# Kernel tuning notes

Measured on AMD Instinct MI355X. Metric: run time of the kernel, lower is better.

The kernel has to match this reference:

```python
import jax, jax.numpy as jnp
import numpy as np

N, M, D, OUT, K, L = 2048, 64, 64, 64, 3, 3  # meta-nodes, subgraph-nodes, channels, out, hops, layers
EPS = 1e-5


def setup_inputs() -> dict:
    key = jax.random.key(0)
    ks = jax.random.split(key, 6)
    x = jax.random.normal(ks[0], (N, M, D), dtype=jnp.float32)
    adj = jax.random.randint(ks[1], (N, N), 0, 2, dtype=jnp.int32)        # meta-graph adjacency
    sub_adj = jax.random.randint(ks[2], (M, M), 0, 2, dtype=jnp.int32)    # per-node subgraph adjacency
    # GCNConv params: (num_layers, k+1 convs per layer, D, D)
    W_convs = jax.random.normal(ks[3], (L, K + 1, D, D), dtype=jnp.float32) / np.float32(np.sqrt(D))
    b_convs = jnp.zeros((L, K + 1, D), dtype=jnp.float32)
    # LayerNorm over the trailing (m, d) dims, per layer
    ln_gamma = jnp.ones((L, M, D), dtype=jnp.float32)
    ln_beta = jnp.zeros((L, M, D), dtype=jnp.float32)
    W_lin = jax.random.normal(ks[4], (M * D, OUT), dtype=jnp.float32) / np.float32(np.sqrt(M * D))
    b_lin = jnp.zeros((OUT,), dtype=jnp.float32)
    return dict(x=x, sub_adj=sub_adj, adj=adj, W_convs=W_convs, b_convs=b_convs,
                ln_gamma=ln_gamma, ln_beta=ln_beta, W_lin=W_lin, b_lin=b_lin)


def _gcn_norm(A):
    # symmetric GCN normalization with self loops: D^{-1/2} (A+I) D^{-1/2}
    A = A.astype(jnp.float32) + jnp.eye(A.shape[0], dtype=jnp.float32)
    dinv = jax.lax.rsqrt(A.sum(axis=1))  # degree >= 1 thanks to self loops
    return dinv[:, None] * A * dinv[None, :]


def reference(x, sub_adj, adj, W_convs, b_convs, ln_gamma, ln_beta, W_lin, b_lin):
    # precompute_adj: dense powers [A, A^2, ..., A^K] of the meta-graph adjacency
    A = adj.astype(jnp.float32)
    cached = [A]
    P = A
    for _ in range(K - 1):
        P = P @ A
        cached.append(P)

    Sn = _gcn_norm(sub_adj)  # (M, M) shared normalized subgraph propagation

    def gcn(h, W, b):
        # GCNConv over the subgraph (m) dimension: Sn @ (h W) + b, batched over n
        return jnp.einsum('uv,nvd->nud', Sn, h @ W) + b

    for l in range(L):
        h = gcn(x, W_convs[l, 0], b_convs[l, 0])  # L[0](x, sub_adj)
        x_i = x
        for i in range(K):
            # k-hop propagation over the meta graph: x_i <- A^i-power @ x_i
            x_i = jnp.einsum('nj,jmd->nmd', cached[i], x_i)
            h = h + gcn(x_i, W_convs[l, i + 1], b_convs[l, i + 1])
        # LayerNorm over trailing (m, d) dims, then ReLU
        mu = h.mean(axis=(1, 2), keepdims=True)
        var = h.var(axis=(1, 2), keepdims=True)
        x = (h - mu) * jax.lax.rsqrt(var + EPS) * ln_gamma[l] + ln_beta[l]
        x = jax.nn.relu(x)

    # final readout linear over flattened (m*d)
    out = x.reshape(N, M * D) @ W_lin + b_lin  # (N, OUT)
    return out
```

## Files before the change

kernel.cpp:

```cpp
#include <hip/hip_runtime.h>
#include <math.h>

#define NN 2048
#define MM 64
#define DD 64
#define MD 4096
#define NLAYER 3
#define EPS 1e-5f

typedef unsigned short u16;
typedef unsigned int u32;
typedef __attribute__((ext_vector_type(8))) short bf16x8;
typedef __attribute__((ext_vector_type(4))) float f32x4;

__device__ inline u16 f32_to_bf16(float f) {
    u32 u = __float_as_uint(f);
    u32 r = (u + 0x7FFFu + ((u >> 16) & 1u)) >> 16;
    return (u16)r;
}
__device__ inline float bf16_to_f32(u16 h) { return __uint_as_float((u32)h << 16); }
__device__ inline void split3(float f, u16& h, u16& l, u16& q) {
    h = f32_to_bf16(f); float r = f - bf16_to_f32(h);
    l = f32_to_bf16(r); r -= bf16_to_f32(l);
    q = f32_to_bf16(r);
}

__global__ __launch_bounds__(256) void aprep_kernel(const int* __restrict__ adj,
                                                    u16* __restrict__ Abf,
                                                    u16* __restrict__ ATbf) {
    __shared__ u16 T[64][65];
    const int r0 = blockIdx.y * 64, c0 = blockIdx.x * 64;
    const int tid = threadIdx.x;
#pragma unroll
    for (int e = 0; e < 16; ++e) {
        int idx = e * 256 + tid;
        int i = idx >> 6, j = idx & 63;
        int a = adj[(long)(r0 + i) * NN + c0 + j];
        u16 b = a ? (u16)0x3F80 : (u16)0;
        Abf[(long)(r0 + i) * NN + c0 + j] = b;
        T[i][j] = b;
    }
    __syncthreads();
#pragma unroll
    for (int e = 0; e < 16; ++e) {
        int idx = e * 256 + tid;
        int cc = idx >> 6, rr = idx & 63;
        ATbf[(long)(c0 + cc) * NN + r0 + rr] = T[rr][cc];
    }
}

__global__ __launch_bounds__(256) void snprep_kernel(const int* __restrict__ sub,
                                                     u16* __restrict__ SnS) {
    __shared__ float dinv[64];
    __shared__ float Snl[64][65];
    int tid = threadIdx.x;
    if (tid < 64) {
        float s = 1.f;
        for (int v = 0; v < 64; ++v) s += (float)sub[tid * 64 + v];
        dinv[tid] = 1.f / sqrtf(s);
    }
    __syncthreads();
    for (int t = tid; t < 4096; t += 256) {
        int u = t >> 6, v = t & 63;
        float a = (float)sub[t] + (u == v ? 1.f : 0.f);
        Snl[u][v] = dinv[u] * a * dinv[v];
    }
    __syncthreads();
    for (int u = tid * 2; u < tid * 2 + 2; ++u) {
        int row = u >> 3, c8 = u & 7;
        int su = (u ^ ((u >> 3) & 7)) * 8;
#pragma unroll
        for (int e = 0; e < 8; ++e) {
            u16 h, l, q; split3(Snl[row][c8 * 8 + e], h, l, q);
            SnS[su + e] = h;
            SnS[4096 + su + e] = l;
            SnS[8192 + su + e] = q;
        }
    }
}

__global__ __launch_bounds__(256) void wprep_kernel(const float* __restrict__ Wc,
                                                    u16* __restrict__ WtS) {
    __shared__ float Wl[64][65];
    const int cu = blockIdx.x, tid = threadIdx.x;
    const float* W = Wc + (size_t)cu * 4096;
    for (int t = tid; t < 4096; t += 256) Wl[t >> 6][t & 63] = W[t];
    __syncthreads();
    u16* dst = WtS + (size_t)cu * 3 * 4096;
    for (int u = tid * 2; u < tid * 2 + 2; ++u) {
        int d = u >> 3, c8 = u & 7;
        int su = (u ^ ((u >> 3) & 7)) * 8;
#pragma unroll
        for (int e = 0; e < 8; ++e) {
            u16 h, l, q; split3(Wl[c8 * 8 + e][d], h, l, q);
            dst[su + e] = h;
            dst[4096 + su + e] = l;
            dst[8192 + su + e] = q;
        }
    }
}

template <int S>
__global__ __launch_bounds__(256) void split_pow_kernel(const float* __restrict__ X,
                                                        u16* __restrict__ P, long n) {
    long i = (long)blockIdx.x * 256 + threadIdx.x;
    if (i >= n) return;
    float v = X[i];
#pragma unroll
    for (int s = 0; s < S; ++s) {
        u16 h = f32_to_bf16(v);
        P[(long)s * n + i] = h;
        v -= bf16_to_f32(h);
    }
}

__global__ __launch_bounds__(256) void split3t_kernel(const float* __restrict__ X,
                                                      u16* __restrict__ P, int R, int Cc) {
    __shared__ float T[64][65];
    const int r0 = blockIdx.y * 64, c0 = blockIdx.x * 64;
    const int tid = threadIdx.x;
#pragma unroll
    for (int e = 0; e < 16; ++e) {
        int idx = e * 256 + tid;
        int i = idx >> 6, j = idx & 63;
        T[i][j] = X[(long)(r0 + i) * Cc + c0 + j];
    }
    __syncthreads();
    const long planeStride = (long)R * Cc;
#pragma unroll
    for (int e = 0; e < 16; ++e) {
        int idx = e * 256 + tid;
        int cc = idx >> 6, rr = idx & 63;
        float v = T[rr][cc];
        u16 h, l, q; split3(v, h, l, q);
        long o = (long)(c0 + cc) * R + r0 + rr;
        P[o] = h;
        P[planeStride + o] = l;
        P[2 * planeStride + o] = q;
    }
}

template <int SP, int SQ, int SMAX>
__global__ __launch_bounds__(256) void gemm_pairs(const u16* __restrict__ Ap, long aStride,
                                                  const u16* __restrict__ Bp, long bStride,
                                                  float* __restrict__ C, int M, int N, int K) {
    __shared__ u16 lds[(SP + SQ) * 4096];
    const int tid = threadIdx.x;
    const int wave = tid >> 6, lane = tid & 63;
    const int nwg = gridDim.x * gridDim.y;
    int bid = blockIdx.y * gridDim.x + blockIdx.x;
    int sbid = (bid & 7) * (nwg >> 3) + (bid >> 3);
    const int bm = (sbid / gridDim.x) * 128, bn = (sbid % gridDim.x) * 128;
    const int wr = (wave >> 1) * 64, wc = (wave & 1) * 64;

    f32x4 acc[4][4];
#pragma unroll
    for (int i = 0; i < 4; ++i)
#pragma unroll
        for (int j = 0; j < 4; ++j) acc[i][j] = (f32x4){0.f, 0.f, 0.f, 0.f};

    const int kb16 = lane >> 4, lr = lane & 15;
    int aoff[4], boff[4];
#pragma unroll
    for (int mi = 0; mi < 4; ++mi) {
        int ua = (wr + mi * 16 + lr) * 4 + kb16;
        aoff[mi] = (ua ^ ((ua >> 3) & 7)) * 16;
        int ub = (wc + mi * 16 + lr) * 4 + kb16;
        boff[mi] = (ub ^ ((ub >> 3) & 7)) * 16;
    }
    auto stage = [&](int k0) {
#pragma unroll
        for (int u8 = 0; u8 < (SP + SQ) * 2; ++u8) {
            int uu = u8 * 4 + wave;
            int p = uu >> 3, i = uu & 7;
            int us = i * 64 + lane;
            int ulin = us ^ ((us >> 3) & 7);
            int r = ulin >> 2, kb = ulin & 3;
            const u16* src; int rowbase;
            if (p < SP) { src = Ap + (long)p * aStride; rowbase = bm; }
            else        { src = Bp + (long)(p - SP) * bStride; rowbase = bn; }
            const char* g = (const char*)src + ((long)(rowbase + r) * K + k0) * 2 + kb * 16;
            char* l = (char*)lds + p * 8192 + i * 1024 + lane * 16;
            __builtin_amdgcn_global_load_lds((const __attribute__((address_space(1))) void*)g,
                                             (__attribute__((address_space(3))) void*)l, 16, 0, 0);
        }
    };
    stage(0);
    __syncthreads();
    for (int k0 = 0; k0 < K; k0 += 32) {
        bf16x8 a[SP][4], b[SQ][4];
#pragma unroll
        for (int s = 0; s < SP; ++s)
#pragma unroll
            for (int mi = 0; mi < 4; ++mi)
                a[s][mi] = *(const bf16x8*)((const char*)lds + s * 8192 + aoff[mi]);
#pragma unroll
        for (int t = 0; t < SQ; ++t)
#pragma unroll
            for (int ni = 0; ni < 4; ++ni)
                b[t][ni] = *(const bf16x8*)((const char*)lds + (SP + t) * 8192 + boff[ni]);
        __syncthreads();
        if (k0 + 32 < K) stage(k0 + 32);
#pragma unroll
        for (int s = 0; s < SP; ++s)
#pragma unroll
            for (int t = 0; t < SQ; ++t)
                if (s + t <= SMAX) {
#pragma unroll
                    for (int mi = 0; mi < 4; ++mi)
#pragma unroll
                        for (int ni = 0; ni < 4; ++ni)
                            acc[mi][ni] = __builtin_amdgcn_mfma_f32_16x16x32_bf16(
                                a[s][mi], b[t][ni], acc[mi][ni], 0, 0, 0);
                }
        __syncthreads();
    }
#pragma unroll
    for (int mi = 0; mi < 4; ++mi)
#pragma unroll
        for (int ni = 0; ni < 4; ++ni)
#pragma unroll
            for (int j = 0; j < 4; ++j)
                C[(long)(bm + wr + mi * 16 + (lane >> 4) * 4 + j) * N + bn + wc + ni * 16 + lr] =
                    acc[mi][ni][j];
}

template <int NC, int MODE>
__global__ __launch_bounds__(256, 2) void gcn_conv_kernel(
    const float* __restrict__ X0, const float* __restrict__ X1,
    const float* __restrict__ X2, const float* __restrict__ X3,
    const u16* __restrict__ WtS,
    const float* __restrict__ bias,
    const u16* __restrict__ SnS,
    const float* __restrict__ gam, const float* __restrict__ bet,
    float* __restrict__ Hout) {
    __shared__ u16 lds[9 * 4096];
    __shared__ float redf[4];
    const int tid = threadIdx.x;
    const int wave = tid >> 6, lane = tid & 63;
    const int lr = lane & 15, lg = lane >> 4;
    const int n = blockIdx.x;
    const int TT = 0, WT = 3 * 4096, SN = 6 * 4096;

    {
        const char* src = (const char*)SnS;
        char* dst = (char*)lds + (size_t)SN * 2;
#pragma unroll
        for (int i = 0; i < 6; ++i)
            __builtin_amdgcn_global_load_lds(
                (const __attribute__((address_space(1))) void*)(src + (i * 256 + tid) * 16),
                (__attribute__((address_space(3))) void*)(dst + (i * 256 + tid) * 16), 16, 0, 0);
    }
    const float* Xc[4] = {X0, X1, X2, X3};
    f32x4 accH[4];
#pragma unroll
    for (int ni = 0; ni < 4; ++ni) accH[ni] = (f32x4){0.f, 0.f, 0.f, 0.f};

    for (int c = 0; c < NC; ++c) {
        __syncthreads();
        {
            const char* wsrc = (const char*)(WtS + (size_t)c * 3 * 4096);
            char* wdst = (char*)lds + (size_t)WT * 2;
#pragma unroll
            for (int i = 0; i < 6; ++i)
                __builtin_amdgcn_global_load_lds(
                    (const __attribute__((address_space(1))) void*)(wsrc + (i * 256 + tid) * 16),
                    (__attribute__((address_space(3))) void*)(wdst + (i * 256 + tid) * 16), 16, 0, 0);
        }
        const float* xp = Xc[c] + (size_t)n * 4096;
        bf16x8 xb[3][4][2];
#pragma unroll
        for (int ni = 0; ni < 4; ++ni)
#pragma unroll
            for (int ks = 0; ks < 2; ++ks) {
                int off = (ni * 16 + lr) * 64 + ks * 32 + lg * 8;
                f32x4 v0 = *(const f32x4*)(xp + off);
                f32x4 v1 = *(const f32x4*)(xp + off + 4);
#pragma unroll
                for (int e = 0; e < 8; ++e) {
                    float f = (e < 4) ? v0[e] : v1[e - 4];
                    u16 h, l, q; split3(f, h, l, q);
                    xb[0][ni][ks][e] = (short)h;
                    xb[1][ni][ks][e] = (short)l;
                    xb[2][ni][ks][e] = (short)q;
                }
            }
        __syncthreads();
        f32x4 accT[4];
#pragma unroll
        for (int ni = 0; ni < 4; ++ni) accT[ni] = (f32x4){0.f, 0.f, 0.f, 0.f};
#pragma unroll
        for (int ks = 0; ks < 2; ++ks) {
            bf16x8 aw[3];
#pragma unroll
            for (int s = 0; s < 3; ++s) {
                int u = (wave * 16 + lr) * 8 + ks * 4 + lg;
                aw[s] = *(const bf16x8*)(lds + WT + s * 4096 + (u ^ ((u >> 3) & 7)) * 8);
            }
#pragma unroll
            for (int ni = 0; ni < 4; ++ni) {
                accT[ni] = __builtin_amdgcn_mfma_f32_16x16x32_bf16(aw[0], xb[0][ni][ks], accT[ni], 0, 0, 0);
                accT[ni] = __builtin_amdgcn_mfma_f32_16x16x32_bf16(aw[0], xb[1][ni][ks], accT[ni], 0, 0, 0);
                accT[ni] = __builtin_amdgcn_mfma_f32_16x16x32_bf16(aw[1], xb[0][ni][ks], accT[ni], 0, 0, 0);
                accT[ni] = __builtin_amdgcn_mfma_f32_16x16x32_bf16(aw[1], xb[1][ni][ks], accT[ni], 0, 0, 0);
                accT[ni] = __builtin_amdgcn_mfma_f32_16x16x32_bf16(aw[2], xb[0][ni][ks], accT[ni], 0, 0, 0);
                accT[ni] = __builtin_amdgcn_mfma_f32_16x16x32_bf16(aw[0], xb[2][ni][ks], accT[ni], 0, 0, 0);
            }
        }
#pragma unroll
        for (int ni = 0; ni < 4; ++ni)
#pragma unroll
            for (int j = 0; j < 4; ++j) {
                int d = wave * 16 + lg * 4 + j;
                int v = ni * 16 + lr;
                u16 h, l, q; split3(accT[ni][j], h, l, q);
                int u = d * 8 + (v >> 3);
                int o = (u ^ ((u >> 3) & 7)) * 8 + (v & 7);
                lds[TT + o] = h;
                lds[TT + 4096 + o] = l;
                lds[TT + 8192 + o] = q;
            }
        __syncthreads();
#pragma unroll
        for (int ks = 0; ks < 2; ++ks) {
            bf16x8 as_[3];
#pragma unroll
            for (int s = 0; s < 3; ++s) {
                int u = (wave * 16 + lr) * 8 + ks * 4 + lg;
                as_[s] = *(const bf16x8*)(lds + SN + s * 4096 + (u ^ ((u >> 3) & 7)) * 8);
            }
#pragma unroll
            for (int ni = 0; ni < 4; ++ni) {
                bf16x8 bt[3];
#pragma unroll
                for (int t = 0; t < 3; ++t) {
                    int u = (ni * 16 + lr) * 8 + ks * 4 + lg;
                    bt[t] = *(const bf16x8*)(lds + TT + t * 4096 + (u ^ ((u >> 3) & 7)) * 8);
                }
                accH[ni] = __builtin_amdgcn_mfma_f32_16x16x32_bf16(as_[0], bt[0], accH[ni], 0, 0, 0);
                accH[ni] = __builtin_amdgcn_mfma_f32_16x16x32_bf16(as_[0], bt[1], accH[ni], 0, 0, 0);
                accH[ni] = __builtin_amdgcn_mfma_f32_16x16x32_bf16(as_[1], bt[0], accH[ni], 0, 0, 0);
                accH[ni] = __builtin_amdgcn_mfma_f32_16x16x32_bf16(as_[1], bt[1], accH[ni], 0, 0, 0);
                accH[ni] = __builtin_amdgcn_mfma_f32_16x16x32_bf16(as_[2], bt[0], accH[ni], 0, 0, 0);
                accH[ni] = __builtin_amdgcn_mfma_f32_16x16x32_bf16(as_[0], bt[2], accH[ni], 0, 0, 0);
            }
        }
#pragma unroll
        for (int ni = 0; ni < 4; ++ni) {
            float bv = bias[c * 64 + ni * 16 + lr];
            accH[ni][0] += bv; accH[ni][1] += bv; accH[ni][2] += bv; accH[ni][3] += bv;
        }
    }
    float* hp = Hout + (size_t)n * 4096;
    float val[4][4];
#pragma unroll
    for (int ni = 0; ni < 4; ++ni)
#pragma unroll
        for (int j = 0; j < 4; ++j) {
            int idx = (wave * 16 + lg * 4 + j) * 64 + ni * 16 + lr;
            float v = accH[ni][j];
            if (MODE == 0 || MODE == 2) v += hp[idx];
            val[ni][j] = v;
        }
    if (MODE == 0 || MODE == 1) {
#pragma unroll
        for (int ni = 0; ni < 4; ++ni)
#pragma unroll
            for (int j = 0; j < 4; ++j)
                hp[(wave * 16 + lg * 4 + j) * 64 + ni * 16 + lr] = val[ni][j];
        return;
    }
    float part = 0.f;
#pragma unroll
    for (int ni = 0; ni < 4; ++ni)
#pragma unroll
        for (int j = 0; j < 4; ++j) part += val[ni][j];
#pragma unroll
    for (int o = 32; o; o >>= 1) part += __shfl_down(part, o);
    if (lane == 0) redf[wave] = part;
    __syncthreads();
    float mean = (redf[0] + redf[1] + redf[2] + redf[3]) * (1.f / 4096.f);
    float p2 = 0.f;
#pragma unroll
    for (int ni = 0; ni < 4; ++ni)
#pragma unroll
        for (int j = 0; j < 4; ++j) {
            float d_ = val[ni][j] - mean;
            p2 += d_ * d_;
        }
#pragma unroll
    for (int o = 32; o; o >>= 1) p2 += __shfl_down(p2, o);
    __syncthreads();
    if (lane == 0) redf[wave] = p2;
    __syncthreads();
    float var = (redf[0] + redf[1] + redf[2] + redf[3]) * (1.f / 4096.f);
    float rstd = 1.f / sqrtf(var + EPS);
#pragma unroll
    for (int ni = 0; ni < 4; ++ni)
#pragma unroll
        for (int j = 0; j < 4; ++j) {
            int idx = (wave * 16 + lg * 4 + j) * 64 + ni * 16 + lr;
            float v = (val[ni][j] - mean) * rstd * gam[idx] + bet[idx];
            hp[idx] = v > 0.f ? v : 0.f;
        }
}

__global__ __launch_bounds__(256) void readout_kernel(const float* __restrict__ X,
                                                      const float* __restrict__ Wl,
                                                      const float* __restrict__ bl,
                                                      float* __restrict__ out) {
    const int n = blockIdx.x;
    const int o = threadIdx.x & 63, c = threadIdx.x >> 6;
    const float* xn = X + (size_t)n * MD;
    float s = 0.f;
    for (int i = c * 1024; i < (c + 1) * 1024; ++i) s += xn[i] * Wl[(size_t)i * 64 + o];
    __shared__ float red[4][64];
    red[c][o] = s;
    __syncthreads();
    if (c == 0) out[(size_t)n * 64 + o] = red[0][o] + red[1][o] + red[2][o] + red[3][o] + bl[o];
}

extern "C" void kernel_launch(void* const* d_in, const int* in_sizes, int n_in,
                              void* d_out, int out_size, void* d_ws, size_t ws_size,
                              hipStream_t stream) {
    const float* x     = (const float*)d_in[0];
    const int*   sub   = (const int*)d_in[1];
    const int*   adj   = (const int*)d_in[2];
    const float* Wc    = (const float*)d_in[3];
    const float* bc    = (const float*)d_in[4];
    const float* gamma = (const float*)d_in[5];
    const float* beta  = (const float*)d_in[6];
    const float* Wlin  = (const float*)d_in[7];
    const float* blin  = (const float*)d_in[8];
    float* out = (float*)d_out;

    char* w = (char*)d_ws;
    u16* Abf = (u16*)w;  w += (size_t)NN * NN * 2;
    u16* A2p = (u16*)w;  w += (size_t)2 * NN * NN * 2;
    u16* A3p = (u16*)w;  w += (size_t)3 * NN * NN * 2;
    u16* SnS = (u16*)w;  w += (size_t)3 * 4096 * 2;
    u16* WtS = (u16*)w;  w += (size_t)12 * 3 * 4096 * 2;
    u16* S   = (u16*)w;  w += (size_t)3 * NN * MD * 2;
    const size_t baseBytes = (size_t)(w - (char*)d_ws);
    const size_t ybytes = (size_t)NN * MD * 4;
    const bool fused = ws_size >= baseBytes + 4 * ybytes;
    u16* ATbf = S;
    float* A2f = (float*)((char*)S + (size_t)NN * NN * 2);
    float* A3f = (float*)((char*)A2f + (size_t)NN * NN * 4);

    aprep_kernel<<<dim3(32, 32), 256, 0, stream>>>(adj, Abf, ATbf);
    snprep_kernel<<<1, 256, 0, stream>>>(sub, SnS);
    wprep_kernel<<<12, 256, 0, stream>>>(Wc, WtS);
    gemm_pairs<1, 1, 2><<<dim3(16, 16), 256, 0, stream>>>(Abf, 0, ATbf, 0, A2f, NN, NN, NN);
    split_pow_kernel<2><<<(NN * NN + 255) / 256, 256, 0, stream>>>(A2f, A2p, (long)NN * NN);
    gemm_pairs<2, 1, 2><<<dim3(16, 16), 256, 0, stream>>>(A2p, (long)NN * NN, ATbf, 0, A3f, NN, NN, NN);
    split_pow_kernel<3><<<(NN * NN + 255) / 256, 256, 0, stream>>>(A3f, A3p, (long)NN * NN);

    const dim3 gp(32, 16);
    if (fused) {
        float* Y[4];
        for (int i = 0; i < 4; ++i) { Y[i] = (float*)w; w += ybytes; }
        const float* xin = x;
        for (int l = 0; l < NLAYER; ++l) {
            float* p1 = Y[l % 4];
            float* p2 = Y[(l + 1) % 4];
            float* p3 = Y[(l + 2) % 4];
            const u16* Wl = WtS + (size_t)l * 12 * 4096;
            split3t_kernel<<<dim3(64, 32), 256, 0, stream>>>(xin, S, NN, MD);
            gemm_pairs<1, 3, 2><<<gp, 256, 0, stream>>>(Abf, 0, S, (long)NN * MD, p1, NN, MD, NN);
            split3t_kernel<<<dim3(64, 32), 256, 0, stream>>>(p1, S, NN, MD);
            gemm_pairs<2, 3, 2><<<gp, 256, 0, stream>>>(A2p, (long)NN * NN, S, (long)NN * MD, p2, NN, MD, NN);
            split3t_kernel<<<dim3(64, 32), 256, 0, stream>>>(p2, S, NN, MD);
            gemm_pairs<3, 3, 2><<<gp, 256, 0, stream>>>(A3p, (long)NN * NN, S, (long)NN * MD, p3, NN, MD, NN);
            gcn_conv_kernel<4, 3><<<NN, 256, 0, stream>>>(xin, p1, p2, p3, Wl,
                bc + (size_t)l * 256, SnS, gamma + (size_t)l * 4096, beta + (size_t)l * 4096, p1);
            xin = p1;
        }
        readout_kernel<<<NN, 256, 0, stream>>>(xin, Wlin, blin, out);
    } else {
        float* Xp = (float*)w; w += ybytes;
        float* H  = (float*)w; w += ybytes;
        const float* xin = x;
        for (int l = 0; l < NLAYER; ++l) {
            const u16* Wl = WtS + (size_t)l * 12 * 4096;
            const float* bl = bc + (size_t)l * 256;
            split3t_kernel<<<dim3(64, 32), 256, 0, stream>>>(xin, S, NN, MD);
            gemm_pairs<1, 3, 2><<<gp, 256, 0, stream>>>(Abf, 0, S, (long)NN * MD, Xp, NN, MD, NN);
            gcn_conv_kernel<1, 1><<<NN, 256, 0, stream>>>(xin, xin, xin, xin, Wl, bl,
                SnS, nullptr, nullptr, H);
            gcn_conv_kernel<1, 0><<<NN, 256, 0, stream>>>(Xp, Xp, Xp, Xp, Wl + 3 * 4096, bl + 64,
                SnS, nullptr, nullptr, H);
            split3t_kernel<<<dim3(64, 32), 256, 0, stream>>>(Xp, S, NN, MD);
            gemm_pairs<2, 3, 2><<<gp, 256, 0, stream>>>(A2p, (long)NN * NN, S, (long)NN * MD, Xp, NN, MD, NN);
            gcn_conv_kernel<1, 0><<<NN, 256, 0, stream>>>(Xp, Xp, Xp, Xp, Wl + 6 * 4096, bl + 128,
                SnS, nullptr, nullptr, H);
            split3t_kernel<<<dim3(64, 32), 256, 0, stream>>>(Xp, S, NN, MD);
            gemm_pairs<3, 3, 2><<<gp, 256, 0, stream>>>(A3p, (long)NN * NN, S, (long)NN * MD, Xp, NN, MD, NN);
            gcn_conv_kernel<1, 2><<<NN, 256, 0, stream>>>(Xp, Xp, Xp, Xp, Wl + 9 * 4096, bl + 192,
                SnS, gamma + (size_t)l * 4096, beta + (size_t)l * 4096, H);
            xin = H;
        }
        readout_kernel<<<NN, 256, 0, stream>>>(xin, Wlin, blin, out);
    }
}
```

Before: 1.963 ms.

## Fuse bf16 split into GEMM epilogues and batch readout rows per block

The GEMM epilogue now writes the 3-way bf16 split of its output directly, optionally transposed, into the operand planes of the next hop. This removes the separate split_pow and split3t kernels between hops and during the adjacency-power precompute. The readout kernel now processes 8 nodes per block and stages W_lin tiles in LDS, so the weight is re-read less often. A new middle workspace tier is added. The costs are a heavier epilogue with scattered 16-bit stores and one more workspace buffer.

```diff
diff --git a/kernel.cpp b/kernel.cpp
--- a/kernel.cpp
+++ b/kernel.cpp
@@ -10,6 +10,7 @@
 
 typedef unsigned short u16;
 typedef unsigned int u32;
+typedef unsigned long long u64;
 typedef __attribute__((ext_vector_type(8))) short bf16x8;
 typedef __attribute__((ext_vector_type(4))) float f32x4;
 
@@ -100,20 +101,6 @@
     }
 }
 
-template <int S>
-__global__ __launch_bounds__(256) void split_pow_kernel(const float* __restrict__ X,
-                                                        u16* __restrict__ P, long n) {
-    long i = (long)blockIdx.x * 256 + threadIdx.x;
-    if (i >= n) return;
-    float v = X[i];
-#pragma unroll
-    for (int s = 0; s < S; ++s) {
-        u16 h = f32_to_bf16(v);
-        P[(long)s * n + i] = h;
-        v -= bf16_to_f32(h);
-    }
-}
-
 __global__ __launch_bounds__(256) void split3t_kernel(const float* __restrict__ X,
                                                       u16* __restrict__ P, int R, int Cc) {
     __shared__ float T[64][65];
@@ -140,10 +127,12 @@
     }
 }
 
-template <int SP, int SQ, int SMAX>
+template <int SP, int SQ, int SMAX, int OSPL, int OTRANS>
 __global__ __launch_bounds__(256) void gemm_pairs(const u16* __restrict__ Ap, long aStride,
                                                   const u16* __restrict__ Bp, long bStride,
-                                                  float* __restrict__ C, int M, int N, int K) {
+                                                  float* __restrict__ C,
+                                                  u16* __restrict__ Sout,
+                                                  int M, int N, int K) {
     __shared__ u16 lds[(SP + SQ) * 4096];
     const int tid = threadIdx.x;
     const int wave = tid >> 6, lane = tid & 63;
@@ -160,6 +149,7 @@
         for (int j = 0; j < 4; ++j) acc[i][j] = (f32x4){0.f, 0.f, 0.f, 0.f};
 
     const int kb16 = lane >> 4, lr = lane & 15;
+    const int lg = lane >> 4;
     int aoff[4], boff[4];
 #pragma unroll
     for (int mi = 0; mi < 4; ++mi) {
@@ -221,8 +211,48 @@
         for (int ni = 0; ni < 4; ++ni)
 #pragma unroll
             for (int j = 0; j < 4; ++j)
-                C[(long)(bm + wr + mi * 16 + (lane >> 4) * 4 + j) * N + bn + wc + ni * 16 + lr] =
+                C[(long)(bm + wr + mi * 16 + lg * 4 + j) * N + bn + wc + ni * 16 + lr] =
                     acc[mi][ni][j];
+    if (OSPL > 0) {
+        const long pe = (long)M * N;
+        if (OTRANS) {
+#pragma unroll
+            for (int ni = 0; ni < 4; ++ni) {
+                long col = bn + wc + ni * 16 + lr;
+#pragma unroll
+                for (int mi = 0; mi < 4; ++mi) {
+                    long row0 = bm + wr + mi * 16 + lg * 4;
+                    u16 hh[4], ll[4], qq[4];
+#pragma unroll
+                    for (int j = 0; j < 4; ++j) split3(acc[mi][ni][j], hh[j], ll[j], qq[j]);
+                    long o = col * M + row0;
+                    *(u64*)(Sout + o) =
+                        (u64)hh[0] | ((u64)hh[1] << 16) | ((u64)hh[2] << 32) | ((u64)hh[3] << 48);
+                    if (OSPL > 1)
+                        *(u64*)(Sout + pe + o) =
+                            (u64)ll[0] | ((u64)ll[1] << 16) | ((u64)ll[2] << 32) | ((u64)ll[3] << 48);
+                    if (OSPL > 2)
+                        *(u64*)(Sout + 2 * pe + o) =
+                            (u64)qq[0] | ((u64)qq[1] << 16) | ((u64)qq[2] << 32) | ((u64)qq[3] << 48);
+                }
+            }
+        } else {
+#pragma unroll
+            for (int mi = 0; mi < 4; ++mi)
+#pragma unroll
+                for (int j = 0; j < 4; ++j) {
+                    long row = bm + wr + mi * 16 + lg * 4 + j;
+#pragma unroll
+                    for (int ni = 0; ni < 4; ++ni) {
+                        long o = row * N + bn + wc + ni * 16 + lr;
+                        u16 h, l, q; split3(acc[mi][ni][j], h, l, q);
+                        Sout[o] = h;
+                        if (OSPL > 1) Sout[pe + o] = l;
+                        if (OSPL > 2) Sout[2 * pe + o] = q;
+                    }
+                }
+        }
+    }
 }
 
 template <int NC, int MODE>
@@ -409,15 +439,39 @@
                                                       const float* __restrict__ Wl,
                                                       const float* __restrict__ bl,
                                                       float* __restrict__ out) {
-    const int n = blockIdx.x;
-    const int o = threadIdx.x & 63, c = threadIdx.x >> 6;
-    const float* xn = X + (size_t)n * MD;
-    float s = 0.f;
-    for (int i = c * 1024; i < (c + 1) * 1024; ++i) s += xn[i] * Wl[(size_t)i * 64 + o];
-    __shared__ float red[4][64];
-    red[c][o] = s;
-    __syncthreads();
-    if (c == 0) out[(size_t)n * 64 + o] = red[0][o] + red[1][o] + red[2][o] + red[3][o] + bl[o];
+    __shared__ float Wls[64][64];
+    __shared__ float red[4][8][64];
+    const int tid = threadIdx.x;
+    const int o = tid & 63, c = tid >> 6;
+    const int n0 = blockIdx.x * 8;
+    float acc[8] = {};
+    const int r = tid >> 2, cq = (tid & 3) * 16;
+    for (int k0 = 0; k0 < 4096; k0 += 64) {
+        __syncthreads();
+        const float* wsrc = Wl + (long)(k0 + r) * 64 + cq;
+        *(f32x4*)&Wls[r][cq + 0]  = *(const f32x4*)(wsrc + 0);
+        *(f32x4*)&Wls[r][cq + 4]  = *(const f32x4*)(wsrc + 4);
+        *(f32x4*)&Wls[r][cq + 8]  = *(const f32x4*)(wsrc + 8);
+        *(f32x4*)&Wls[r][cq + 12] = *(const f32x4*)(wsrc + 12);
+        __syncthreads();
+#pragma unroll
+        for (int i = 0; i < 8; ++i) {
+            const float* xr = X + (long)(n0 + i) * 4096 + k0 + c * 16;
+            float s = acc[i];
+#pragma unroll
+            for (int kk = 0; kk < 16; ++kk) s += xr[kk] * Wls[c * 16 + kk][o];
+            acc[i] = s;
+        }
+    }
+#pragma unroll
+    for (int i = 0; i < 8; ++i) red[c][i][o] = acc[i];
+    __syncthreads();
+    if (c == 0) {
+#pragma unroll
+        for (int i = 0; i < 8; ++i)
+            out[(long)(n0 + i) * 64 + o] =
+                red[0][i][o] + red[1][i][o] + red[2][i][o] + red[3][i][o] + bl[o];
+    }
 }
 
 extern "C" void kernel_launch(void* const* d_in, const int* in_sizes, int n_in,
@@ -440,66 +494,109 @@
     u16* A3p = (u16*)w;  w += (size_t)3 * NN * NN * 2;
     u16* SnS = (u16*)w;  w += (size_t)3 * 4096 * 2;
     u16* WtS = (u16*)w;  w += (size_t)12 * 3 * 4096 * 2;
-    u16* S   = (u16*)w;  w += (size_t)3 * NN * MD * 2;
     const size_t baseBytes = (size_t)(w - (char*)d_ws);
+    const size_t sbytes = (size_t)3 * NN * MD * 2;
     const size_t ybytes = (size_t)NN * MD * 4;
-    const bool fused = ws_size >= baseBytes + 4 * ybytes;
-    u16* ATbf = S;
-    float* A2f = (float*)((char*)S + (size_t)NN * NN * 2);
-    float* A3f = (float*)((char*)A2f + (size_t)NN * NN * 4);
+    const long sPlane = (long)NN * MD;
+
+    u16* S0 = (u16*)w;
+    u16* ATbf = S0;
+
+    const size_t needA = baseBytes + 2 * sbytes + 4 * ybytes;
+    const size_t needB = baseBytes + 2 * sbytes + 3 * ybytes;
+    int tier = (ws_size >= needA) ? 0 : (ws_size >= needB) ? 1 : 2;
+
+    float* Cscr = (tier == 2) ? (float*)((char*)S0 + sbytes)
+                              : (float*)((char*)S0 + 2 * sbytes);
 
     aprep_kernel<<<dim3(32, 32), 256, 0, stream>>>(adj, Abf, ATbf);
     snprep_kernel<<<1, 256, 0, stream>>>(sub, SnS);
     wprep_kernel<<<12, 256, 0, stream>>>(Wc, WtS);
-    gemm_pairs<1, 1, 2><<<dim3(16, 16), 256, 0, stream>>>(Abf, 0, ATbf, 0, A2f, NN, NN, NN);
-    split_pow_kernel<2><<<(NN * NN + 255) / 256, 256, 0, stream>>>(A2f, A2p, (long)NN * NN);
-    gemm_pairs<2, 1, 2><<<dim3(16, 16), 256, 0, stream>>>(A2p, (long)NN * NN, ATbf, 0, A3f, NN, NN, NN);
-    split_pow_kernel<3><<<(NN * NN + 255) / 256, 256, 0, stream>>>(A3f, A3p, (long)NN * NN);
+    gemm_pairs<1, 1, 2, 2, 0><<<dim3(16, 16), 256, 0, stream>>>(
+        Abf, 0, ATbf, 0, Cscr, A2p, NN, NN, NN);
+    gemm_pairs<2, 1, 2, 3, 0><<<dim3(16, 16), 256, 0, stream>>>(
+        A2p, (long)NN * NN, ATbf, 0, Cscr, A3p, NN, NN, NN);
 
     const dim3 gp(32, 16);
-    if (fused) {
+    if (tier == 0) {
+        u16* S1 = S0 + (size_t)3 * sPlane;
         float* Y[4];
-        for (int i = 0; i < 4; ++i) { Y[i] = (float*)w; w += ybytes; }
+        char* yw = (char*)S1 + sbytes;
+        for (int i = 0; i < 4; ++i) { Y[i] = (float*)yw; yw += ybytes; }
         const float* xin = x;
         for (int l = 0; l < NLAYER; ++l) {
             float* p1 = Y[l % 4];
             float* p2 = Y[(l + 1) % 4];
             float* p3 = Y[(l + 2) % 4];
             const u16* Wl = WtS + (size_t)l * 12 * 4096;
-            split3t_kernel<<<dim3(64, 32), 256, 0, stream>>>(xin, S, NN, MD);
-            gemm_pairs<1, 3, 2><<<gp, 256, 0, stream>>>(Abf, 0, S, (long)NN * MD, p1, NN, MD, NN);
-            split3t_kernel<<<dim3(64, 32), 256, 0, stream>>>(p1, S, NN, MD);
-            gemm_pairs<2, 3, 2><<<gp, 256, 0, stream>>>(A2p, (long)NN * NN, S, (long)NN * MD, p2, NN, MD, NN);
-            split3t_kernel<<<dim3(64, 32), 256, 0, stream>>>(p2, S, NN, MD);
-            gemm_pairs<3, 3, 2><<<gp, 256, 0, stream>>>(A3p, (long)NN * NN, S, (long)NN * MD, p3, NN, MD, NN);
+            split3t_kernel<<<dim3(64, 32), 256, 0, stream>>>(xin, S0, NN, MD);
+            gemm_pairs<1, 3, 2, 3, 1><<<gp, 256, 0, stream>>>(
+                Abf, 0, S0, sPlane, p1, S1, NN, MD, NN);
+            gemm_pairs<2, 3, 2, 3, 1><<<gp, 256, 0, stream>>>(
+                A2p, (long)NN * NN, S1, sPlane, p2, S0, NN, MD, NN);
+            gemm_pairs<3, 3, 2, 0, 0><<<gp, 256, 0, stream>>>(
+                A3p, (long)NN * NN, S0, sPlane, p3, nullptr, NN, MD, NN);
             gcn_conv_kernel<4, 3><<<NN, 256, 0, stream>>>(xin, p1, p2, p3, Wl,
                 bc + (size_t)l * 256, SnS, gamma + (size_t)l * 4096, beta + (size_t)l * 4096, p1);
             xin = p1;
         }
-        readout_kernel<<<NN, 256, 0, stream>>>(xin, Wlin, blin, out);
+        readout_kernel<<<NN / 8, 256, 0, stream>>>(xin, Wlin, blin, out);
+    } else if (tier == 1) {
+        u16* S1 = S0 + (size_t)3 * sPlane;
+        char* yw = (char*)S1 + sbytes;
+        float* Xa = (float*)yw; yw += ybytes;
+        float* Ha = (float*)yw; yw += ybytes;
+        float* Hb = (float*)yw; yw += ybytes;
+        const float* xin = x;
+        for (int l = 0; l < NLAYER; ++l) {
+            float* H = (l & 1) ? Hb : Ha;
+            const u16* Wl = WtS + (size_t)l * 12 * 4096;
+            const float* bl = bc + (size_t)l * 256;
+            split3t_kernel<<<dim3(64, 32), 256, 0, stream>>>(xin, S0, NN, MD);
+            gcn_conv_kernel<1, 1><<<NN, 256, 0, stream>>>(xin, xin, xin, xin, Wl, bl,
+                SnS, nullptr, nullptr, H);
+            gemm_pairs<1, 3, 2, 3, 1><<<gp, 256, 0, stream>>>(
+                Abf, 0, S0, sPlane, Xa, S1, NN, MD, NN);
+            gcn_conv_kernel<1, 0><<<NN, 256, 0, stream>>>(Xa, Xa, Xa, Xa, Wl + 3 * 4096, bl + 64,
+                SnS, nullptr, nullptr, H);
+            gemm_pairs<2, 3, 2, 3, 1><<<gp, 256, 0, stream>>>(
+                A2p, (long)NN * NN, S1, sPlane, Xa, S0, NN, MD, NN);
+            gcn_conv_kernel<1, 0><<<NN, 256, 0, stream>>>(Xa, Xa, Xa, Xa, Wl + 6 * 4096, bl + 128,
+                SnS, nullptr, nullptr, H);
+            gemm_pairs<3, 3, 2, 0, 0><<<gp, 256, 0, stream>>>(
+                A3p, (long)NN * NN, S0, sPlane, Xa, nullptr, NN, MD, NN);
+            gcn_conv_kernel<1, 2><<<NN, 256, 0, stream>>>(Xa, Xa, Xa, Xa, Wl + 9 * 4096, bl + 192,
+                SnS, gamma + (size_t)l * 4096, beta + (size_t)l * 4096, H);
+            xin = H;
+        }
+        readout_kernel<<<NN / 8, 256, 0, stream>>>(xin, Wlin, blin, out);
     } else {
-        float* Xp = (float*)w; w += ybytes;
-        float* H  = (float*)w; w += ybytes;
+        char* yw = (char*)S0 + sbytes;
+        float* Xp = (float*)yw; yw += ybytes;
+        float* H  = (float*)yw; yw += ybytes;
         const float* xin = x;
         for (int l = 0; l < NLAYER; ++l) {
             const u16* Wl = WtS + (size_t)l * 12 * 4096;
             const float* bl = bc + (size_t)l * 256;
-            split3t_kernel<<<dim3(64, 32), 256, 0, stream>>>(xin, S, NN, MD);
-            gemm_pairs<1, 3, 2><<<gp, 256, 0, stream>>>(Abf, 0, S, (long)NN * MD, Xp, NN, MD, NN);
+            split3t_kernel<<<dim3(64, 32), 256, 0, stream>>>(xin, S0, NN, MD);
+            gemm_pairs<1, 3, 2, 0, 0><<<gp, 256, 0, stream>>>(
+                Abf, 0, S0, sPlane, Xp, nullptr, NN, MD, NN);
             gcn_conv_kernel<1, 1><<<NN, 256, 0, stream>>>(xin, xin, xin, xin, Wl, bl,
                 SnS, nullptr, nullptr, H);
             gcn_conv_kernel<1, 0><<<NN, 256, 0, stream>>>(Xp, Xp, Xp, Xp, Wl + 3 * 4096, bl + 64,
                 SnS, nullptr, nullptr, H);
-            split3t_kernel<<<dim3(64, 32), 256, 0, stream>>>(Xp, S, NN, MD);
-            gemm_pairs<2, 3, 2><<<gp, 256, 0, stream>>>(A2p, (long)NN * NN, S, (long)NN * MD, Xp, NN, MD, NN);
+            split3t_kernel<<<dim3(64, 32), 256, 0, stream>>>(Xp, S0, NN, MD);
+            gemm_pairs<2, 3, 2, 0, 0><<<gp, 256, 0, stream>>>(
+                A2p, (long)NN * NN, S0, sPlane, Xp, nullptr, NN, MD, NN);
             gcn_conv_kernel<1, 0><<<NN, 256, 0, stream>>>(Xp, Xp, Xp, Xp, Wl + 6 * 4096, bl + 128,
                 SnS, nullptr, nullptr, H);
-            split3t_kernel<<<dim3(64, 32), 256, 0, stream>>>(Xp, S, NN, MD);
-            gemm_pairs<3, 3, 2><<<gp, 256, 0, stream>>>(A3p, (long)NN * NN, S, (long)NN * MD, Xp, NN, MD, NN);
+            split3t_kernel<<<dim3(64, 32), 256, 0, stream>>>(Xp, S0, NN, MD);
+            gemm_pairs<3, 3, 2, 0, 0><<<gp, 256, 0, stream>>>(
+                A3p, (long)NN * NN, S0, sPlane, Xp, nullptr, NN, MD, NN);
             gcn_conv_kernel<1, 2><<<NN, 256, 0, stream>>>(Xp, Xp, Xp, Xp, Wl + 9 * 4096, bl + 192,
                 SnS, gamma + (size_t)l * 4096, beta + (size_t)l * 4096, H);
             xin = H;
         }
-        readout_kernel<<<NN, 256, 0, stream>>>(xin, Wlin, blin, out);
-    }
-}
+        readout_kernel<<<NN / 8, 256, 0, stream>>>(xin, Wlin, blin, out);
+    }
+}
```

Result: faster. 1.925 ms (-2.0%).
